# Kernel tuning notes

Measured on AMD Instinct MI355X. Metric: run time of the kernel, lower is better.

The kernel has to match this reference:

```python
import jax, jax.numpy as jnp
import numpy as np

# unit constants from Converter._set_unit (astropy values, precomputed):
# unit_nu_f_nu = Lsun / (4*pi*(10 pc)^2) in erg/s/cm^2
UNIT_NU_F_NU = 3.1995e-07
# unit_f_nu = unit_nu_f_nu / (c / angstrom) in Jy
UNIT_F_NU = 1.0673e-02


def setup_inputs() -> dict:
    key = jax.random.key(0)
    k1, k2 = jax.random.split(key)
    B, F, L = 8192, 128, 8192
    # strictly increasing wavelength grid in Angstrom
    lam = 100.0 + 6.0 * (jnp.arange(L, dtype=jnp.float32) + 1.0)
    # positive fluxes so log10 is defined
    l_target = jax.random.uniform(k1, (B, L), dtype=jnp.float32) + 0.1
    # filter transmissions (already unit-normalized in __init__); keep positive
    trans_filter = 1e-3 * (jax.random.uniform(k2, (F, L), dtype=jnp.float32) + 0.01)
    return {"l_target": l_target, "trans_filter": trans_filter, "lam": lam, "return_ph": 1}


def reference(l_target, trans_filter, lam, return_ph):
    if return_ph:
        # trapz(y, x) == sum_l y[l] * w[l] with trapezoid weights w from lam.
        dx = jnp.diff(lam)  # [L-1]
        w = jnp.zeros_like(lam).at[:-1].add(0.5 * dx).at[1:].add(0.5 * dx)  # [L]
        # fuse weights into the filter matrix -> single GEMM, no [B,F,L] intermediate
        wt = trans_filter * w[None, :]  # [F, L]
        flux = jnp.einsum('bl,fl->bf', l_target, wt)  # [B, F]
        return -2.5 * jnp.log10(flux)
    else:
        return l_target * lam[None, :] * UNIT_F_NU
```

## Files before the change

### kernel.cpp

```cpp
#include <hip/hip_runtime.h>
#include <hip/hip_bf16.h>
#include <cstdint>

#define B_ROWS 8192
#define F_FILT 128
#define L_LEN  8192
#define SPLITK 16
#define KCHUNK (L_LEN / SPLITK)
#define STEPS  (KCHUNK / 32)
#define WM     16
#define WAVES  2
#define BM     (WM * WAVES)
#define MBLK   (B_ROWS / BM)

typedef __attribute__((ext_vector_type(4))) float f32x4;
typedef __attribute__((ext_vector_type(8))) short bf16x8;

__device__ __forceinline__ short f2bf(float f) {
  union { float f; unsigned u; } v; v.f = f;
  unsigned u = v.u + 0x7FFFu + ((v.u >> 16) & 1u);
  return (short)(u >> 16);
}

__device__ __forceinline__ bf16x8 cvt8(f32x4 x, f32x4 y) {
  bf16x8 r;
  r[0] = f2bf(x[0]); r[1] = f2bf(x[1]); r[2] = f2bf(x[2]); r[3] = f2bf(x[3]);
  r[4] = f2bf(y[0]); r[5] = f2bf(y[1]); r[6] = f2bf(y[2]); r[7] = f2bf(y[3]);
  return r;
}

__global__ void build_wt(const float* __restrict__ trans,
                         const float* __restrict__ lam,
                         ushort* __restrict__ bp) {
  int o = blockIdx.x * blockDim.x + threadIdx.x;
  int lane = o & 63, j = (o >> 6) & 7, gs = o >> 9;
  int f = j * 16 + (lane & 15);
  int k = gs * 32 + (lane >> 4) * 8;
  bf16x8 h;
#pragma unroll
  for (int i = 0; i < 8; ++i) {
    int l = k + i;
    float lo = (l > 0)         ? lam[l - 1] : lam[0];
    float hi = (l < L_LEN - 1) ? lam[l + 1] : lam[L_LEN - 1];
    h[i] = f2bf(trans[(size_t)f * L_LEN + l] * (0.5f * (hi - lo)));
  }
  *(bf16x8*)(bp + (size_t)o * 8) = h;
}

__global__ __launch_bounds__(128, 4)
void gemm_splitk(const float* __restrict__ A,
                 const ushort* __restrict__ BP,
                 float* __restrict__ P ) {
  const int lane = threadIdx.x & 63;
  const int wave = threadIdx.x >> 6;
  const int rl = lane & 15;
  const int kg = lane >> 4;
  const int m0 = blockIdx.x * BM + wave * WM;
  const int s  = blockIdx.y;
  const int k0 = s * KCHUNK;

  const float*  pa = A  + (size_t)(m0 + rl) * L_LEN + k0 + kg * 8;
  const ushort* pb = BP + ((size_t)(k0 / 32) * 512 + lane) * 8;

  f32x4 acc[8] = {};

  f32x4 an0 = *(const f32x4*)pa;
  f32x4 an1 = *(const f32x4*)(pa + 4);

#pragma unroll
  for (int st = 0; st < STEPS; ++st) {
    f32x4 ac0 = an0, ac1 = an1;
    if (st + 1 < STEPS) {
      const float* p = pa + (st + 1) * 32;
      an0 = *(const f32x4*)p;
      an1 = *(const f32x4*)(p + 4);
    }
    bf16x8 af = cvt8(ac0, ac1);
    const ushort* pbs = pb + (size_t)st * 4096;
#pragma unroll
    for (int j = 0; j < 8; ++j) {
      bf16x8 b = *(const bf16x8*)(pbs + (size_t)j * 512);
      acc[j] = __builtin_amdgcn_mfma_f32_16x16x32_bf16(af, b, acc[j], 0, 0, 0);
    }
  }

  float* po = P + ((size_t)s * B_ROWS + m0) * F_FILT;
#pragma unroll
  for (int r = 0; r < 4; ++r) {
    const int row = kg * 4 + r;
#pragma unroll
    for (int j = 0; j < 8; ++j)
      po[(size_t)row * F_FILT + j * 16 + rl] = acc[j][r];
  }
}

__global__ void finish(const float* __restrict__ P, float* __restrict__ out) {
  int idx = blockIdx.x * blockDim.x + threadIdx.x;
  float s = 0.f;
#pragma unroll
  for (int i = 0; i < SPLITK; ++i)
    s += P[(size_t)i * ((size_t)B_ROWS * F_FILT) + idx];
  out[idx] = -2.5f * log10f(s);
}

extern "C" void kernel_launch(void* const* d_in, const int* in_sizes, int n_in,
                              void* d_out, int out_size, void* d_ws, size_t ws_size,
                              hipStream_t stream) {
  const float* A    = (const float*)d_in[0];
  const float* T    = (const float*)d_in[1];
  const float* lam  = (const float*)d_in[2];

  ushort* bp = (ushort*)d_ws;
  float*  P  = (float*)((char*)d_ws + (size_t)F_FILT * L_LEN * sizeof(ushort));
  float*  out = (float*)d_out;

  build_wt<<<(F_FILT * L_LEN / 8) / 256, 256, 0, stream>>>(T, lam, bp);
  gemm_splitk<<<dim3(MBLK, SPLITK), 128, 0, stream>>>(A, bp, P);
  finish<<<(B_ROWS * F_FILT) / 256, 256, 0, stream>>>(P, out);
}
```

Measured before the change: 425.1 us.

## Use packed bf16 convert, 32-bit offsets, higher occupancy and vectorized finish

Swaps the software round-to-nearest bf16 conversion for the hardware v_cvt_pk_bf16_f32 instruction via inline asm. Switches A/B addressing to 32-bit offsets to cut 64-bit address math, and splits the B-fragment loop into two halves. Raises the launch-bounds occupancy hint from 4 to 8 blocks per SM, which may force fewer registers. Vectorizes the split-K reduction kernel to float4 loads and stores with a quarter of the threads.

Result: no change. 422.7 us (-0.6%).

```diff
diff --git a/kernel.cpp b/kernel.cpp
--- a/kernel.cpp
+++ b/kernel.cpp
@@ -23,10 +23,12 @@
 }
 
 __device__ __forceinline__ bf16x8 cvt8(f32x4 x, f32x4 y) {
-  bf16x8 r;
-  r[0] = f2bf(x[0]); r[1] = f2bf(x[1]); r[2] = f2bf(x[2]); r[3] = f2bf(x[3]);
-  r[4] = f2bf(y[0]); r[5] = f2bf(y[1]); r[6] = f2bf(y[2]); r[7] = f2bf(y[3]);
-  return r;
+  union { unsigned u[4]; bf16x8 v; } r;
+  asm("v_cvt_pk_bf16_f32 %0, %1, %2" : "=v"(r.u[0]) : "v"(x[0]), "v"(x[1]));
+  asm("v_cvt_pk_bf16_f32 %0, %1, %2" : "=v"(r.u[1]) : "v"(x[2]), "v"(x[3]));
+  asm("v_cvt_pk_bf16_f32 %0, %1, %2" : "=v"(r.u[2]) : "v"(y[0]), "v"(y[1]));
+  asm("v_cvt_pk_bf16_f32 %0, %1, %2" : "=v"(r.u[3]) : "v"(y[2]), "v"(y[3]));
+  return r.v;
 }
 
 __global__ void build_wt(const float* __restrict__ trans,
@@ -47,7 +49,7 @@
   *(bf16x8*)(bp + (size_t)o * 8) = h;
 }
 
-__global__ __launch_bounds__(128, 4)
+__global__ __launch_bounds__(128, 8)
 void gemm_splitk(const float* __restrict__ A,
                  const ushort* __restrict__ BP,
                  float* __restrict__ P ) {
@@ -59,28 +61,33 @@
   const int s  = blockIdx.y;
   const int k0 = s * KCHUNK;
 
-  const float*  pa = A  + (size_t)(m0 + rl) * L_LEN + k0 + kg * 8;
-  const ushort* pb = BP + ((size_t)(k0 / 32) * 512 + lane) * 8;
+  const uint32_t aoff = (uint32_t)(m0 + rl) * L_LEN + (uint32_t)k0 + (uint32_t)kg * 8;
+  const uint32_t boff = ((uint32_t)(k0 / 32) * 512u + (uint32_t)lane) * 8u;
 
   f32x4 acc[8] = {};
 
-  f32x4 an0 = *(const f32x4*)pa;
-  f32x4 an1 = *(const f32x4*)(pa + 4);
+  f32x4 an0 = *(const f32x4*)(A + aoff);
+  f32x4 an1 = *(const f32x4*)(A + aoff + 4);
 
 #pragma unroll
   for (int st = 0; st < STEPS; ++st) {
     f32x4 ac0 = an0, ac1 = an1;
     if (st + 1 < STEPS) {
-      const float* p = pa + (st + 1) * 32;
-      an0 = *(const f32x4*)p;
-      an1 = *(const f32x4*)(p + 4);
+      an0 = *(const f32x4*)(A + aoff + (st + 1) * 32);
+      an1 = *(const f32x4*)(A + aoff + (st + 1) * 32 + 4);
     }
     bf16x8 af = cvt8(ac0, ac1);
-    const ushort* pbs = pb + (size_t)st * 4096;
+    const ushort* pbs0 = BP + boff + (size_t)st * 4096;
+    const ushort* pbs1 = pbs0 + 2048;
 #pragma unroll
-    for (int j = 0; j < 8; ++j) {
-      bf16x8 b = *(const bf16x8*)(pbs + (size_t)j * 512);
+    for (int j = 0; j < 4; ++j) {
+      bf16x8 b = *(const bf16x8*)(pbs0 + j * 512);
       acc[j] = __builtin_amdgcn_mfma_f32_16x16x32_bf16(af, b, acc[j], 0, 0, 0);
+    }
+#pragma unroll
+    for (int j = 0; j < 4; ++j) {
+      bf16x8 b = *(const bf16x8*)(pbs1 + j * 512);
+      acc[4 + j] = __builtin_amdgcn_mfma_f32_16x16x32_bf16(af, b, acc[4 + j], 0, 0, 0);
     }
   }
 
@@ -95,12 +102,19 @@
 }
 
 __global__ void finish(const float* __restrict__ P, float* __restrict__ out) {
-  int idx = blockIdx.x * blockDim.x + threadIdx.x;
-  float s = 0.f;
+  int t = blockIdx.x * blockDim.x + threadIdx.x;
+  f32x4 s = {};
 #pragma unroll
-  for (int i = 0; i < SPLITK; ++i)
-    s += P[(size_t)i * ((size_t)B_ROWS * F_FILT) + idx];
-  out[idx] = -2.5f * log10f(s);
+  for (int i = 0; i < SPLITK; ++i) {
+    f32x4 p = *(const f32x4*)(P + (size_t)i * ((size_t)B_ROWS * F_FILT) + (size_t)t * 4);
+    s[0] += p[0]; s[1] += p[1]; s[2] += p[2]; s[3] += p[3];
+  }
+  f32x4 o;
+  o[0] = -2.5f * log10f(s[0]);
+  o[1] = -2.5f * log10f(s[1]);
+  o[2] = -2.5f * log10f(s[2]);
+  o[3] = -2.5f * log10f(s[3]);
+  *(f32x4*)(out + (size_t)t * 4) = o;
 }
 
 extern "C" void kernel_launch(void* const* d_in, const int* in_sizes, int n_in,
@@ -116,5 +130,5 @@
 
   build_wt<<<(F_FILT * L_LEN / 8) / 256, 256, 0, stream>>>(T, lam, bp);
   gemm_splitk<<<dim3(MBLK, SPLITK), 128, 0, stream>>>(A, bp, P);
-  finish<<<(B_ROWS * F_FILT) / 256, 256, 0, stream>>>(P, out);
+  finish<<<(B_ROWS * F_FILT / 4) / 256, 256, 0, stream>>>(P, out);
 }
```
